# Performance work log

Measured on AMD Instinct MI355X. Metric: run time of the kernel, lower is better.

## Reference

```python
import jax, jax.numpy as jnp
import numpy as np

N, E = 50000, 500000          # nodes per type, edges per message type
F_IN, H, L = 128, 128, 8      # input feat, hidden_size, num_labels
EPS, SLOPE = 1e-5, 0.01       # BatchNorm eps, LeakyReLU slope


def setup_inputs() -> dict:
    key = jax.random.key(0)
    ks = jax.random.split(key, 16)
    s = 0.05
    d = {}
    d["x_n0"] = jax.random.normal(ks[0], (N, F_IN), jnp.float32)
    d["x_n1"] = jax.random.normal(ks[1], (N, F_IN), jnp.float32)
    # stacked per-message-type SAGE params (3 message types), two layers
    d["Wn1"] = jax.random.normal(ks[2], (3, F_IN, H), jnp.float32) * s
    d["Ws1"] = jax.random.normal(ks[3], (3, F_IN, H), jnp.float32) * s
    d["Wu1"] = jax.random.normal(ks[4], (3, 2 * H, H), jnp.float32) * s
    d["Wn2"] = jax.random.normal(ks[5], (3, H, H), jnp.float32) * s
    d["Ws2"] = jax.random.normal(ks[6], (3, H, H), jnp.float32) * s
    d["Wu2"] = jax.random.normal(ks[7], (3, 2 * H, H), jnp.float32) * s
    for nm in ("bn1", "bs1", "bu1", "bn2", "bs2", "bu2"):
        d[nm] = jnp.zeros((3, H), jnp.float32)
    # per-node-type BatchNorm affine params (2 node types), two layers
    d["gamma1"] = jnp.ones((2, H), jnp.float32)
    d["beta1"] = jnp.zeros((2, H), jnp.float32)
    d["gamma2"] = jnp.ones((2, H), jnp.float32)
    d["beta2"] = jnp.zeros((2, H), jnp.float32)
    # per-node-type post-MP linear
    d["Wp"] = jax.random.normal(ks[8], (2, H, L), jnp.float32) * s
    d["bp"] = jnp.zeros((2, L), jnp.float32)
    # edge_index per message type: [2, E] with row0=src, row1=dst
    d["ei0"] = jax.random.randint(ks[9], (2, E), 0, N, jnp.int32)   # n0 -> n1
    d["ei1"] = jax.random.randint(ks[10], (2, E), 0, N, jnp.int32)  # n1 -> n0
    d["ei2"] = jax.random.randint(ks[11], (2, E), 0, N, jnp.int32)  # n0 -> n0
    return d


def _segment_mean(x, idx, n):
    s = jax.ops.segment_sum(x, idx, num_segments=n)
    c = jax.ops.segment_sum(jnp.ones((idx.shape[0], 1), x.dtype), idx, num_segments=n)
    return s / jnp.maximum(c, 1.0)


def _sage(x_src, x_dst, ei, Wn, bn, Ws, bs, Wu, bu):
    # gather source feats per edge, scatter-mean to dst, then linear branches
    agg = _segment_mean(x_src[ei[0]], ei[1], x_dst.shape[0])  # [N_dst, F]
    h = jnp.concatenate([agg @ Wn + bn, x_dst @ Ws + bs], axis=-1)
    return h @ Wu + bu


def _bn(x, g, b):
    m = x.mean(0)
    v = ((x - m) ** 2).mean(0)  # biased variance, as torch BN training mode
    return (x - m) * jax.lax.rsqrt(v + EPS) * g + b


def _lrelu(x):
    return jnp.where(x >= 0, x, SLOPE * x)


def _layer(x0, x1, ei0, ei1, ei2, Wn, bn, Ws, bs, Wu, bu, gamma, beta):
    m0 = _sage(x0, x1, ei0, Wn[0], bn[0], Ws[0], bs[0], Wu[0], bu[0])  # dst n1
    m1 = _sage(x1, x0, ei1, Wn[1], bn[1], Ws[1], bs[1], Wu[1], bu[1])  # dst n0
    m2 = _sage(x0, x0, ei2, Wn[2], bn[2], Ws[2], bs[2], Wu[2], bu[2])  # dst n0
    h0 = 0.5 * (m1 + m2)   # mean over the 2 message types targeting n0
    h1 = m0                # single message type for n1
    h0 = _lrelu(_bn(h0, gamma[0], beta[0]))
    h1 = _lrelu(_bn(h1, gamma[1], beta[1]))
    return h0, h1


def reference(x_n0, x_n1, Wn1, bn1, Ws1, bs1, Wu1, bu1,
              Wn2, bn2, Ws2, bs2, Wu2, bu2,
              gamma1, beta1, gamma2, beta2, Wp, bp, ei0, ei1, ei2):
    h0, h1 = _layer(x_n0, x_n1, ei0, ei1, ei2, Wn1, bn1, Ws1, bs1, Wu1, bu1, gamma1, beta1)
    h0, h1 = _layer(h0, h1, ei0, ei1, ei2, Wn2, bn2, Ws2, bs2, Wu2, bu2, gamma2, beta2)
    out0 = h0 @ Wp[0] + bp[0]
    out1 = h1 @ Wp[1] + bp[1]
    return jnp.stack([out0, out1])  # [2, N, L]
```

## Files before the change

kernel.cpp:

```cpp
#include <hip/hip_runtime.h>

#define LBL 8
#define NBMAX 128
#define BSH 9
#define BCAP 8192

typedef __attribute__((ext_vector_type(8))) short short8;
typedef __attribute__((ext_vector_type(4))) float f32x4;

__device__ __forceinline__ uint f2bf(float x) {
    uint u = __float_as_uint(x);
    return (u + 0x7fffu + ((u >> 16) & 1u)) >> 16;
}
__device__ __forceinline__ float bflo(uint v) { return __uint_as_float(v << 16); }
__device__ __forceinline__ float bfhi(uint v) { return __uint_as_float(v & 0xffff0000u); }

__global__ void f2b2(const float4* __restrict__ x0, const float4* __restrict__ x1,
                     uint2* __restrict__ o0, uint2* __restrict__ o1, int n4) {
    int y = blockIdx.y;
    const float4* in = y ? x1 : x0;
    uint2* out = y ? o1 : o0;
    int i = blockIdx.x * blockDim.x + threadIdx.x;
    int stride = gridDim.x * blockDim.x;
    for (; i < n4; i += stride) {
        float4 v = in[i];
        uint2 o;
        o.x = f2bf(v.x) | (f2bf(v.y) << 16);
        o.y = f2bf(v.z) | (f2bf(v.w) << 16);
        out[i] = o;
    }
}


__global__ void bhist3(const int* __restrict__ e0, const int* __restrict__ e1,
                       const int* __restrict__ e2, int E, int NB, int* __restrict__ bcnt) {
    int m = blockIdx.y;
    const int* dst = (m == 0 ? e0 : (m == 1 ? e1 : e2)) + E;
    __shared__ int h[NBMAX];
    int tid = threadIdx.x;
    if (tid < NB) h[tid] = 0;
    __syncthreads();
    int i = blockIdx.x * blockDim.x + tid, st = gridDim.x * blockDim.x;
    for (; i < E; i += st) atomicAdd(&h[dst[i] >> BSH], 1);
    __syncthreads();
    if (tid < NB && h[tid]) atomicAdd(&bcnt[m * NB + tid], h[tid]);
}

__global__ void bscan(const int* __restrict__ bcnt, int* __restrict__ bso,
                      int* __restrict__ gcur, int NB) {
    int m = threadIdx.x;
    if (m >= 3) return;
    int acc = 0;
    for (int b = 0; b < NB; ++b) {
        bso[m * (NB + 1) + b] = acc;
        gcur[m * NB + b] = acc;
        acc += bcnt[m * NB + b];
    }
    bso[m * (NB + 1) + NB] = acc;
}

#define BIN_CH 16
__global__ __launch_bounds__(256) void bin3(const int* __restrict__ e0, const int* __restrict__ e1,
                                            const int* __restrict__ e2, int E, int NB,
                                            int* __restrict__ gcur, int2* __restrict__ pairs) {
    int m = blockIdx.y;
    const int* eb = (m == 0 ? e0 : (m == 1 ? e1 : e2));
    const int* src = eb;
    const int* dst = eb + E;
    int2* pp = pairs + (size_t)m * E;
    int* gc = gcur + m * NB;
    __shared__ int h[NBMAX], base[NBMAX], pos[NBMAX];
    int tid = threadIdx.x;
    if (tid < NB) { h[tid] = 0; pos[tid] = 0; }
    __syncthreads();
    int i0 = blockIdx.x * (256 * BIN_CH);
    int sv[BIN_CH], dv[BIN_CH], bk[BIN_CH];
    #pragma unroll
    for (int u = 0; u < BIN_CH; ++u) {
        int i = i0 + u * 256 + tid;
        bk[u] = -1;
        if (i < E) {
            sv[u] = src[i];
            dv[u] = dst[i];
            bk[u] = dv[u] >> BSH;
            atomicAdd(&h[bk[u]], 1);
        }
    }
    __syncthreads();
    if (tid < NB && h[tid]) base[tid] = atomicAdd(&gc[tid], h[tid]);
    __syncthreads();
    #pragma unroll
    for (int u = 0; u < BIN_CH; ++u) {
        if (bk[u] >= 0) {
            int p = base[bk[u]] + atomicAdd(&pos[bk[u]], 1);
            pp[p] = make_int2(sv[u], dv[u]);
        }
    }
}

__global__ __launch_bounds__(256) void csr3(const int2* __restrict__ pairs, const int* __restrict__ bso,
                                            int E, int N, int NB,
                                            int* __restrict__ offs, int* __restrict__ srcs) {
    int m = blockIdx.y, b = blockIdx.x;
    const int2* pp = pairs + (size_t)m * E;
    int gstart = bso[m * (NB + 1) + b];
    int gend = bso[m * (NB + 1) + b + 1];
    int cnt = gend - gstart;
    if (cnt > BCAP) cnt = BCAP;
    int d0 = b << BSH;
    int dcnt = N - d0;
    if (dcnt > (1 << BSH)) dcnt = 1 << BSH;

    __shared__ int hist[1 << BSH], po[1 << BSH], off0[1 << BSH];
    __shared__ int lsort[BCAP];
    __shared__ int wsum[4];
    int tid = threadIdx.x;
    hist[tid] = 0;
    hist[tid + 256] = 0;
    __syncthreads();
    for (int i = tid; i < cnt; i += 256) atomicAdd(&hist[pp[gstart + i].y - d0], 1);
    __syncthreads();
    int a = hist[2 * tid], b2 = hist[2 * tid + 1];
    int s = a + b2;
    int lane = tid & 63, w = tid >> 6;
    #pragma unroll
    for (int o = 1; o < 64; o <<= 1) {
        int v = __shfl_up(s, o, 64);
        if (lane >= o) s += v;
    }
    if (lane == 63) wsum[w] = s;
    __syncthreads();
    int wp = 0;
    #pragma unroll
    for (int q = 0; q < 4; ++q)
        if (q < w) wp += wsum[q];
    int excl = wp + s - a - b2;
    off0[2 * tid] = excl; off0[2 * tid + 1] = excl + a;
    po[2 * tid] = excl;   po[2 * tid + 1] = excl + a;
    __syncthreads();
    for (int j = tid; j < dcnt; j += 256) offs[(size_t)m * (N + 1) + d0 + j] = gstart + off0[j];
    if (b == NB - 1 && tid == 0) offs[(size_t)m * (N + 1) + N] = bso[m * (NB + 1) + NB];
    for (int i = tid; i < cnt; i += 256) {
        int2 e = pp[gstart + i];
        int p = atomicAdd(&po[e.y - d0], 1);
        if (p < BCAP) lsort[p] = e.x;
    }
    __syncthreads();
    for (int i = tid; i < cnt; i += 256) srcs[(size_t)m * E + gstart + i] = lsort[i];
}

__global__ void agg3(const ushort* __restrict__ s0, const ushort* __restrict__ s1,
                     const ushort* __restrict__ s2,
                     uint* __restrict__ o0, uint* __restrict__ o1, uint* __restrict__ o2,
                     const int* __restrict__ offs, const int* __restrict__ srcs,
                     int n, int E) {
    int m = blockIdx.y;
    const uint4* x = (const uint4*)(m == 0 ? s0 : (m == 1 ? s1 : s2));
    uint4* o = (uint4*)(m == 0 ? o0 : (m == 1 ? o1 : o2));
    const int* off = offs + (size_t)m * (n + 1);
    const int* sl = srcs + (size_t)m * E;

    int tid = threadIdx.x;
    int l16 = tid & 15;
    int row = blockIdx.x * 16 + (tid >> 4);
    if (row >= n) return;
    int s = off[row], e = off[row + 1];
    float a0 = 0, a1 = 0, a2 = 0, a3 = 0, a4 = 0, a5 = 0, a6 = 0, a7 = 0;
    int i = s;
    for (; i + 1 < e; i += 2) {
        uint4 v0 = x[(size_t)sl[i] * 16 + l16];
        uint4 v1 = x[(size_t)sl[i + 1] * 16 + l16];
        a0 += bflo(v0.x) + bflo(v1.x); a1 += bfhi(v0.x) + bfhi(v1.x);
        a2 += bflo(v0.y) + bflo(v1.y); a3 += bfhi(v0.y) + bfhi(v1.y);
        a4 += bflo(v0.z) + bflo(v1.z); a5 += bfhi(v0.z) + bfhi(v1.z);
        a6 += bflo(v0.w) + bflo(v1.w); a7 += bfhi(v0.w) + bfhi(v1.w);
    }
    if (i < e) {
        uint4 v0 = x[(size_t)sl[i] * 16 + l16];
        a0 += bflo(v0.x); a1 += bfhi(v0.x);
        a2 += bflo(v0.y); a3 += bfhi(v0.y);
        a4 += bflo(v0.z); a5 += bfhi(v0.z);
        a6 += bflo(v0.w); a7 += bfhi(v0.w);
    }
    int d = e - s;
    float inv = 1.f / (float)(d > 0 ? d : 1);
    uint4 r;
    r.x = f2bf(a0 * inv) | (f2bf(a1 * inv) << 16);
    r.y = f2bf(a2 * inv) | (f2bf(a3 * inv) << 16);
    r.z = f2bf(a4 * inv) | (f2bf(a5 * inv) << 16);
    r.w = f2bf(a6 * inv) | (f2bf(a7 * inv) << 16);
    o[(size_t)row * 16 + l16] = r;
}

__global__ void fuseW(const float* __restrict__ Wn1, const float* __restrict__ Ws1,
                      const float* __restrict__ Wu1,
                      const float* __restrict__ Wn2, const float* __restrict__ Ws2,
                      const float* __restrict__ Wu2, ushort* __restrict__ FT) {
    int j5 = blockIdx.y;
    int l = j5 / 5, t = j5 - l * 5;
    const float* Wn = l ? Wn2 : Wn1;
    const float* Ws = l ? Ws2 : Ws1;
    const float* Wu = l ? Wu2 : Wu1;
    const float *A0, *B0, *A1 = nullptr, *B1 = nullptr;
    float al;
    switch (t) {
        case 0: A0 = Wn;          B0 = Wu;          al = 1.0f; break;
        case 1: A0 = Wn + 16384;  B0 = Wu + 32768;  al = 0.5f; break;
        case 2: A0 = Wn + 32768;  B0 = Wu + 65536;  al = 0.5f; break;
        case 3: A0 = Ws;          B0 = Wu + 16384;  al = 1.0f; break;
        default:
            A0 = Ws + 16384; B0 = Wu + 49152;
            A1 = Ws + 32768; B1 = Wu + 81920;
            al = 0.5f; break;
    }
    int i = blockIdx.x, j = threadIdx.x;
    float s0 = 0, s1 = 0, s2 = 0, s3 = 0;
    #pragma unroll 4
    for (int k = 0; k < 128; k += 4) {
        s0 += A0[i * 128 + k]     * B0[k * 128 + j];
        s1 += A0[i * 128 + k + 1] * B0[(k + 1) * 128 + j];
        s2 += A0[i * 128 + k + 2] * B0[(k + 2) * 128 + j];
        s3 += A0[i * 128 + k + 3] * B0[(k + 3) * 128 + j];
    }
    if (A1) {
        #pragma unroll 4
        for (int k = 0; k < 128; k += 4) {
            s0 += A1[i * 128 + k]     * B1[k * 128 + j];
            s1 += A1[i * 128 + k + 1] * B1[(k + 1) * 128 + j];
            s2 += A1[i * 128 + k + 2] * B1[(k + 2) * 128 + j];
            s3 += A1[i * 128 + k + 3] * B1[(k + 3) * 128 + j];
        }
    }
    float r = al * ((s0 + s1) + (s2 + s3));
    FT[(size_t)j5 * 16384 + j * 128 + i] = (ushort)f2bf(r);
}

__global__ void fuseB(const float* __restrict__ bn1, const float* __restrict__ bs1,
                      const float* __restrict__ bu1, const float* __restrict__ Wu1,
                      const float* __restrict__ bn2, const float* __restrict__ bs2,
                      const float* __restrict__ bu2, const float* __restrict__ Wu2,
                      float* __restrict__ FC) {
    int jb = blockIdx.x;
    int l = jb >> 1, which = jb & 1;
    const float* bn = l ? bn2 : bn1;
    const float* bs = l ? bs2 : bs1;
    const float* bu = l ? bu2 : bu1;
    const float* Wu = l ? Wu2 : Wu1;
    int j = threadIdx.x;
    float s = 0.f;
    if (which == 0) {
        s = bu[j];
        for (int k = 0; k < 128; ++k)
            s += bn[k] * Wu[k * 128 + j] + bs[k] * Wu[(128 + k) * 128 + j];
    } else {
        #pragma unroll
        for (int tt = 1; tt <= 2; ++tt) {
            const float* Wt = Wu + tt * 32768;
            float p = bu[tt * 128 + j];
            for (int k = 0; k < 128; ++k)
                p += bn[tt * 128 + k] * Wt[k * 128 + j] + bs[tt * 128 + k] * Wt[(128 + k) * 128 + j];
            s += 0.5f * p;
        }
    }
    FC[jb * 128 + j] = s;
}

__global__ __launch_bounds__(256) void gemm2_mfma(
    const ushort* __restrict__ Aq0, const ushort* __restrict__ Wq0,
    const ushort* __restrict__ Aq1, const ushort* __restrict__ Wq1,
    const ushort* __restrict__ Ap0, const ushort* __restrict__ Wp0,
    const ushort* __restrict__ Ap1, const ushort* __restrict__ Wp1,
    const ushort* __restrict__ Ap2, const ushort* __restrict__ Wp2,
    const float* __restrict__ biasq, const float* __restrict__ biasp,
    ushort* __restrict__ Cq, ushort* __restrict__ Cp, int M,
    float* __restrict__ STW) {
    __shared__ ushort As[64 * 128];
    int y = blockIdx.y;
    const float* bias = y ? biasp : biasq;
    ushort* C = y ? Cp : Cq;
    float* colsum = STW + (size_t)(blockIdx.x & 31) * 512 + (y ? 0 : 256);
    float* colsq = colsum + 128;

    int tid = threadIdx.x;
    int wid = tid >> 6;
    int lane = tid & 63;
    int l15 = lane & 15, lg = lane >> 4;
    int row0 = blockIdx.x * 64;
    int nIn = y ? 3 : 2;

    short8 bw[3][4][2];
    #pragma unroll
    for (int inp = 0; inp < 3; ++inp) {
        const ushort* W = (inp == 0) ? (y ? Wp0 : Wq0)
                        : (inp == 1) ? (y ? Wp1 : Wq1) : Wp2;
        #pragma unroll
        for (int k0 = 0; k0 < 4; ++k0)
            #pragma unroll
            for (int cb = 0; cb < 2; ++cb)
                bw[inp][k0][cb] = *(const short8*)(W + (size_t)(wid * 32 + cb * 16 + l15) * 128 + k0 * 32 + lg * 8);
    }

    f32x4 acc[4][2];
    #pragma unroll
    for (int rb = 0; rb < 4; ++rb)
        #pragma unroll
        for (int cb = 0; cb < 2; ++cb) acc[rb][cb] = (f32x4){0.f, 0.f, 0.f, 0.f};

    int r_ = tid >> 4, ch = tid & 15;
    #pragma unroll
    for (int inp = 0; inp < 3; ++inp) {
        if (inp == 2 && nIn == 2) break;
        const ushort* A = (inp == 0) ? (y ? Ap0 : Aq0)
                        : (inp == 1) ? (y ? Ap1 : Aq1) : Ap2;
        __syncthreads();
        #pragma unroll
        for (int p = 0; p < 4; ++p) {
            int row = p * 16 + r_;
            int gr = row0 + row;
            if (gr > M - 1) gr = M - 1;
            uint4 v = *(const uint4*)(A + (size_t)gr * 128 + ch * 8);
            *(uint4*)&As[row * 128 + ((ch ^ (row & 7)) * 8)] = v;
        }
        __syncthreads();
        #pragma unroll
        for (int k0 = 0; k0 < 4; ++k0) {
            short8 a[4];
            #pragma unroll
            for (int rb = 0; rb < 4; ++rb)
                a[rb] = *(const short8*)&As[(rb * 16 + l15) * 128 + (((k0 * 4 + lg) ^ (l15 & 7)) * 8)];
            #pragma unroll
            for (int rb = 0; rb < 4; ++rb)
                #pragma unroll
                for (int cb = 0; cb < 2; ++cb)
                    acc[rb][cb] = __builtin_amdgcn_mfma_f32_16x16x32_bf16(a[rb], bw[inp][k0][cb], acc[rb][cb], 0, 0, 0);
        }
    }

    float ps[2] = {0.f, 0.f}, pq[2] = {0.f, 0.f};
    int colbase = wid * 32;
    #pragma unroll
    for (int cb = 0; cb < 2; ++cb) {
        int col = colbase + cb * 16 + l15;
        float b = bias[col];
        #pragma unroll
        for (int rb = 0; rb < 4; ++rb) {
            int rbase = row0 + rb * 16 + lg * 4;
            #pragma unroll
            for (int i = 0; i < 4; ++i) {
                int r = rbase + i;
                if (r < M) {
                    float v = acc[rb][cb][i] + b;
                    C[(size_t)r * 128 + col] = (ushort)f2bf(v);
                    ps[cb] += v;
                    pq[cb] += v * v;
                }
            }
        }
    }
    #pragma unroll
    for (int cb = 0; cb < 2; ++cb) {
        ps[cb] += __shfl_xor(ps[cb], 16, 64);
        ps[cb] += __shfl_xor(ps[cb], 32, 64);
        pq[cb] += __shfl_xor(pq[cb], 16, 64);
        pq[cb] += __shfl_xor(pq[cb], 32, 64);
    }
    if (lane < 16) {
        atomicAdd(&colsum[colbase + lane], ps[0]);
        atomicAdd(&colsq[colbase + lane], pq[0]);
        atomicAdd(&colsum[colbase + 16 + lane], ps[1]);
        atomicAdd(&colsq[colbase + 16 + lane], pq[1]);
    }
}

__global__ void bn_fin2(float* __restrict__ STW, float* __restrict__ ST,
                        const float* __restrict__ g0, const float* __restrict__ b0,
                        const float* __restrict__ g1, const float* __restrict__ b1, int N) {
    int tid = threadIdx.x;
    int which = tid >> 7, c = tid & 127;
    float s = 0.f, q = 0.f;
    #pragma unroll 8
    for (int cp = 0; cp < 32; ++cp) {
        s += STW[(size_t)cp * 512 + which * 256 + c];
        q += STW[(size_t)cp * 512 + which * 256 + 128 + c];
    }
    #pragma unroll 8
    for (int cp = 0; cp < 32; ++cp) {
        STW[(size_t)cp * 512 + which * 256 + c] = 0.f;
        STW[(size_t)cp * 512 + which * 256 + 128 + c] = 0.f;
    }
    const float* g = which ? g1 : g0;
    const float* b = which ? b1 : b0;
    float m = s / (float)N;
    float v = q / (float)N - m * m;
    float rs = rsqrtf(v + 1e-5f);
    float sc = g[c] * rs;
    ST[512 + which * 256 + c] = sc;
    ST[640 + which * 256 + c] = b[c] - m * sc;
}

__global__ void bn_apply2(const ushort* __restrict__ Cp, ushort* __restrict__ X0b,
                          const ushort* __restrict__ Cq, ushort* __restrict__ X1b,
                          const float* __restrict__ ST, int n4) {
    int y = blockIdx.y;
    const uint2* in = (const uint2*)(y ? Cq : Cp);
    uint2* out = (uint2*)(y ? X1b : X0b);
    const float* sc = ST + 512 + y * 256;
    const float* sh = sc + 128;
    int i = blockIdx.x * blockDim.x + threadIdx.x;
    int stride = gridDim.x * blockDim.x;
    for (; i < n4; i += stride) {
        uint2 v = in[i];
        int cb = (i * 4) & 127;
        float4 s4 = *(const float4*)&sc[cb];
        float4 h4 = *(const float4*)&sh[cb];
        float y0 = bflo(v.x) * s4.x + h4.x;
        float y1 = bfhi(v.x) * s4.y + h4.y;
        float y2 = bflo(v.y) * s4.z + h4.z;
        float y3 = bfhi(v.y) * s4.w + h4.w;
        y0 = (y0 >= 0.f) ? y0 : 0.01f * y0;
        y1 = (y1 >= 0.f) ? y1 : 0.01f * y1;
        y2 = (y2 >= 0.f) ? y2 : 0.01f * y2;
        y3 = (y3 >= 0.f) ? y3 : 0.01f * y3;
        uint2 o;
        o.x = f2bf(y0) | (f2bf(y1) << 16);
        o.y = f2bf(y2) | (f2bf(y3) << 16);
        out[i] = o;
    }
}

__global__ void projbn2(const ushort* __restrict__ Cp, const ushort* __restrict__ Cq,
                        const float* __restrict__ ST,
                        const float* __restrict__ Wp, const float* __restrict__ bp,
                        float* __restrict__ out, int N) {
    int y = blockIdx.y;
    const uint* h = (const uint*)(y ? Cq : Cp);
    const float* W = Wp + y * 1024;
    const float* b = bp + y * 8;
    float* op = out + (size_t)y * N * 8;
    __shared__ float Wsh[1024];
    __shared__ float scs[128], shs[128];
    __shared__ float bsh[8];
    int tid = threadIdx.x;
    for (int i = tid; i < 1024; i += 256) Wsh[i] = W[i];
    if (tid < 128) {
        scs[tid] = ST[512 + y * 256 + tid];
        shs[tid] = ST[640 + y * 256 + tid];
    }
    if (tid < 8) bsh[tid] = b[tid];
    __syncthreads();
    int idx = blockIdx.x * 256 + tid;
    if (idx >= N * LBL) return;
    int r = idx >> 3, c = idx & 7;
    const uint* hr = h + (size_t)r * 64;
    float s = bsh[c];
    #pragma unroll
    for (int k2 = 0; k2 < 64; ++k2) {
        uint v = hr[k2];
        float xa = bflo(v) * scs[2 * k2] + shs[2 * k2];
        float xb = bfhi(v) * scs[2 * k2 + 1] + shs[2 * k2 + 1];
        xa = (xa >= 0.f) ? xa : 0.01f * xa;
        xb = (xb >= 0.f) ? xb : 0.01f * xb;
        s += xa * Wsh[(2 * k2) * 8 + c] + xb * Wsh[(2 * k2 + 1) * 8 + c];
    }
    op[idx] = s;
}


extern "C" void kernel_launch(void* const* d_in, const int* in_sizes, int n_in,
                              void* d_out, int out_size, void* d_ws, size_t ws_size,
                              hipStream_t stream) {
    const float* x0 = (const float*)d_in[0];
    const float* x1 = (const float*)d_in[1];
    const float* Wn1 = (const float*)d_in[2];
    const float* Ws1 = (const float*)d_in[3];
    const float* Wu1 = (const float*)d_in[4];
    const float* Wn2 = (const float*)d_in[5];
    const float* Ws2 = (const float*)d_in[6];
    const float* Wu2 = (const float*)d_in[7];
    const float* bnn[2] = {(const float*)d_in[8], (const float*)d_in[11]};
    const float* bss[2] = {(const float*)d_in[9], (const float*)d_in[12]};
    const float* buu[2] = {(const float*)d_in[10], (const float*)d_in[13]};
    const float* gam[2] = {(const float*)d_in[14], (const float*)d_in[16]};
    const float* bet[2] = {(const float*)d_in[15], (const float*)d_in[17]};
    const float* Wp = (const float*)d_in[18];
    const float* bp = (const float*)d_in[19];
    const int* ei[3] = {(const int*)d_in[20], (const int*)d_in[21], (const int*)d_in[22]};

    const int N = in_sizes[0] / 128;
    const int E = in_sizes[20] / 2;
    const int NB = (N + (1 << BSH) - 1) >> BSH;
    float* out = (float*)d_out;

    char* wp_ = (char*)d_ws;
    auto carve = [&](size_t bytes) {
        char* r = wp_;
        wp_ += (bytes + 255) & ~(size_t)255;
        return r;
    };
    size_t nodeB = (size_t)N * 128 * sizeof(ushort);
    ushort* Cp = (ushort*)carve(nodeB);
    ushort* Cq = (ushort*)carve(nodeB);
    ushort* Pb = (ushort*)carve(nodeB);
    ushort* Rb = (ushort*)carve(nodeB);
    ushort* Sb = (ushort*)carve(nodeB);
    ushort* X0b = (ushort*)carve(nodeB);
    ushort* X1b = (ushort*)carve(nodeB);
    ushort* x0b = (ushort*)carve(nodeB);
    ushort* x1b = (ushort*)carve(nodeB);
    ushort* FT = (ushort*)carve(10 * 16384 * 2);
    float* FC = (float*)carve(4 * 128 * 4);
    float* ST = (float*)carve(1024 * 4);
    float* STW = (float*)carve(32 * 512 * 4);
    int* offs = (int*)carve((size_t)3 * (N + 1) * 4);
    int* srcs = (int*)carve((size_t)3 * E * 4);
    int* bcnt = (int*)carve((size_t)3 * NB * 4);
    int* bso = (int*)carve((size_t)3 * (NB + 1) * 4);
    int* gcur = (int*)carve((size_t)3 * NB * 4);
    int2* pairs = (int2*)Cp;

    const int ag = (N + 15) / 16;
    const int gg = (N + 63) / 64;
    const int pg = (N * LBL + 255) / 256;
    const int bg = (E + 256 * BIN_CH - 1) / (256 * BIN_CH);

    f2b2<<<dim3(1024, 2), 256, 0, stream>>>((const float4*)x0, (const float4*)x1,
                                            (uint2*)x0b, (uint2*)x1b, N * 32);

    hipMemsetAsync(bcnt, 0, (size_t)3 * NB * 4, stream);
    hipMemsetAsync(STW, 0, 32 * 512 * 4, stream);
    bhist3<<<dim3(512, 3), 256, 0, stream>>>(ei[0], ei[1], ei[2], E, NB, bcnt);
    bscan<<<1, 64, 0, stream>>>(bcnt, bso, gcur, NB);
    bin3<<<dim3(bg, 3), 256, 0, stream>>>(ei[0], ei[1], ei[2], E, NB, gcur, pairs);
    csr3<<<dim3(NB, 3), 256, 0, stream>>>(pairs, bso, E, N, NB, offs, srcs);

    fuseW<<<dim3(128, 10), 128, 0, stream>>>(Wn1, Ws1, Wu1, Wn2, Ws2, Wu2, FT);
    fuseB<<<4, 128, 0, stream>>>(bnn[0], bss[0], buu[0], Wu1, bnn[1], bss[1], buu[1], Wu2, FC);

    const ushort* srcS[2][3] = {{x0b, x1b, x0b}, {X0b, X1b, X0b}};
    const ushort* dstX[2][2] = {{x0b, x1b}, {X0b, X1b}};

    for (int l = 0; l < 2; ++l) {
        const ushort* FA0T = FT + (size_t)(l * 5 + 0) * 16384;
        const ushort* FA1T = FT + (size_t)(l * 5 + 1) * 16384;
        const ushort* FA2T = FT + (size_t)(l * 5 + 2) * 16384;
        const ushort* FB1T = FT + (size_t)(l * 5 + 3) * 16384;
        const ushort* FB0T = FT + (size_t)(l * 5 + 4) * 16384;
        const float* fcH1 = FC + (l * 2 + 0) * 128;
        const float* fcH0 = FC + (l * 2 + 1) * 128;

        agg3<<<dim3(ag, 3), 256, 0, stream>>>(srcS[l][0], srcS[l][1], srcS[l][2],
                                              (uint*)Pb, (uint*)Rb, (uint*)Sb,
                                              offs, srcs, N, E);

        gemm2_mfma<<<dim3(gg, 2), 256, 0, stream>>>(
            Pb, FA0T, dstX[l][1], FB1T,
            Rb, FA1T, Sb, FA2T, dstX[l][0], FB0T,
            fcH1, fcH0, Cq, Cp, N, STW);

        bn_fin2<<<1, 256, 0, stream>>>(STW, ST, gam[l], bet[l], gam[l] + 128, bet[l] + 128, N);
        if (l == 0)
            bn_apply2<<<dim3(1024, 2), 256, 0, stream>>>(Cp, X0b, Cq, X1b, ST, N * 32);
    }

    projbn2<<<dim3(pg, 2), 256, 0, stream>>>(Cp, Cq, ST, Wp, bp, out, N);
}
```

Before: 316.0 us.

## Fuse neighbor mean-aggregation into the SAGE MFMA GEMM kernel

Removes the separate agg3 kernel and performs the CSR gather-mean directly into the GEMM's shared-memory A tile. This avoids writing three aggregated node buffers to global memory and reading them back, and saves one launch per layer. The gather loop is unrolled by 4 for more loads in flight, and weight fragments are loaded per input so fewer registers are live. The gather now runs at GEMM occupancy with only 64 rows per block, which may expose more memory latency than the standalone aggregation kernel did.

```diff
diff --git a/kernel.cpp b/kernel.cpp
--- a/kernel.cpp
+++ b/kernel.cpp
@@ -147,49 +147,6 @@
     }
     __syncthreads();
     for (int i = tid; i < cnt; i += 256) srcs[(size_t)m * E + gstart + i] = lsort[i];
-}
-
-__global__ void agg3(const ushort* __restrict__ s0, const ushort* __restrict__ s1,
-                     const ushort* __restrict__ s2,
-                     uint* __restrict__ o0, uint* __restrict__ o1, uint* __restrict__ o2,
-                     const int* __restrict__ offs, const int* __restrict__ srcs,
-                     int n, int E) {
-    int m = blockIdx.y;
-    const uint4* x = (const uint4*)(m == 0 ? s0 : (m == 1 ? s1 : s2));
-    uint4* o = (uint4*)(m == 0 ? o0 : (m == 1 ? o1 : o2));
-    const int* off = offs + (size_t)m * (n + 1);
-    const int* sl = srcs + (size_t)m * E;
-
-    int tid = threadIdx.x;
-    int l16 = tid & 15;
-    int row = blockIdx.x * 16 + (tid >> 4);
-    if (row >= n) return;
-    int s = off[row], e = off[row + 1];
-    float a0 = 0, a1 = 0, a2 = 0, a3 = 0, a4 = 0, a5 = 0, a6 = 0, a7 = 0;
-    int i = s;
-    for (; i + 1 < e; i += 2) {
-        uint4 v0 = x[(size_t)sl[i] * 16 + l16];
-        uint4 v1 = x[(size_t)sl[i + 1] * 16 + l16];
-        a0 += bflo(v0.x) + bflo(v1.x); a1 += bfhi(v0.x) + bfhi(v1.x);
-        a2 += bflo(v0.y) + bflo(v1.y); a3 += bfhi(v0.y) + bfhi(v1.y);
-        a4 += bflo(v0.z) + bflo(v1.z); a5 += bfhi(v0.z) + bfhi(v1.z);
-        a6 += bflo(v0.w) + bflo(v1.w); a7 += bfhi(v0.w) + bfhi(v1.w);
-    }
-    if (i < e) {
-        uint4 v0 = x[(size_t)sl[i] * 16 + l16];
-        a0 += bflo(v0.x); a1 += bfhi(v0.x);
-        a2 += bflo(v0.y); a3 += bfhi(v0.y);
-        a4 += bflo(v0.z); a5 += bfhi(v0.z);
-        a6 += bflo(v0.w); a7 += bfhi(v0.w);
-    }
-    int d = e - s;
-    float inv = 1.f / (float)(d > 0 ? d : 1);
-    uint4 r;
-    r.x = f2bf(a0 * inv) | (f2bf(a1 * inv) << 16);
-    r.y = f2bf(a2 * inv) | (f2bf(a3 * inv) << 16);
-    r.z = f2bf(a4 * inv) | (f2bf(a5 * inv) << 16);
-    r.w = f2bf(a6 * inv) | (f2bf(a7 * inv) << 16);
-    o[(size_t)row * 16 + l16] = r;
 }
 
 __global__ void fuseW(const float* __restrict__ Wn1, const float* __restrict__ Ws1,
@@ -265,14 +222,14 @@
     FC[jb * 128 + j] = s;
 }
 
-__global__ __launch_bounds__(256) void gemm2_mfma(
-    const ushort* __restrict__ Aq0, const ushort* __restrict__ Wq0,
-    const ushort* __restrict__ Aq1, const ushort* __restrict__ Wq1,
-    const ushort* __restrict__ Ap0, const ushort* __restrict__ Wp0,
-    const ushort* __restrict__ Ap1, const ushort* __restrict__ Wp1,
-    const ushort* __restrict__ Ap2, const ushort* __restrict__ Wp2,
+__global__ __launch_bounds__(256) void sage_fused(
+    const ushort* __restrict__ Gq, const ushort* __restrict__ Dq,
+    const ushort* __restrict__ Gp0, const ushort* __restrict__ Gp1,
+    const ushort* __restrict__ Dp,
+    const ushort* __restrict__ FTl,
+    const int* __restrict__ offs, const int* __restrict__ srcs, int E, int M,
     const float* __restrict__ biasq, const float* __restrict__ biasp,
-    ushort* __restrict__ Cq, ushort* __restrict__ Cp, int M,
+    ushort* __restrict__ Cq, ushort* __restrict__ Cp,
     float* __restrict__ STW) {
     __shared__ ushort As[64 * 128];
     int y = blockIdx.y;
@@ -286,40 +243,84 @@
     int lane = tid & 63;
     int l15 = lane & 15, lg = lane >> 4;
     int row0 = blockIdx.x * 64;
-    int nIn = y ? 3 : 2;
-
-    short8 bw[3][4][2];
+    int rloc = tid >> 4, ch = tid & 15;
+
+    f32x4 acc[4][2];
+    #pragma unroll
+    for (int rb = 0; rb < 4; ++rb)
+        #pragma unroll
+        for (int cb = 0; cb < 2; ++cb) acc[rb][cb] = (f32x4){0.f, 0.f, 0.f, 0.f};
+
     #pragma unroll
     for (int inp = 0; inp < 3; ++inp) {
-        const ushort* W = (inp == 0) ? (y ? Wp0 : Wq0)
-                        : (inp == 1) ? (y ? Wp1 : Wq1) : Wp2;
+        if (inp == 2 && y == 0) break;
+        int t = (y == 0) ? (inp == 0 ? 0 : 3) : (inp == 2 ? 4 : inp + 1);
+        bool gath = (y == 0) ? (inp == 0) : (inp < 2);
+        const ushort* W = FTl + (size_t)t * 16384;
+
+        short8 bw[4][2];
         #pragma unroll
         for (int k0 = 0; k0 < 4; ++k0)
             #pragma unroll
             for (int cb = 0; cb < 2; ++cb)
-                bw[inp][k0][cb] = *(const short8*)(W + (size_t)(wid * 32 + cb * 16 + l15) * 128 + k0 * 32 + lg * 8);
-    }
-
-    f32x4 acc[4][2];
-    #pragma unroll
-    for (int rb = 0; rb < 4; ++rb)
-        #pragma unroll
-        for (int cb = 0; cb < 2; ++cb) acc[rb][cb] = (f32x4){0.f, 0.f, 0.f, 0.f};
-
-    int r_ = tid >> 4, ch = tid & 15;
-    #pragma unroll
-    for (int inp = 0; inp < 3; ++inp) {
-        if (inp == 2 && nIn == 2) break;
-        const ushort* A = (inp == 0) ? (y ? Ap0 : Aq0)
-                        : (inp == 1) ? (y ? Ap1 : Aq1) : Ap2;
+                bw[k0][cb] = *(const short8*)(W + (size_t)(wid * 32 + cb * 16 + l15) * 128 + k0 * 32 + lg * 8);
+
         __syncthreads();
-        #pragma unroll
-        for (int p = 0; p < 4; ++p) {
-            int row = p * 16 + r_;
-            int gr = row0 + row;
-            if (gr > M - 1) gr = M - 1;
-            uint4 v = *(const uint4*)(A + (size_t)gr * 128 + ch * 8);
-            *(uint4*)&As[row * 128 + ((ch ^ (row & 7)) * 8)] = v;
+        if (gath) {
+            int m = (y == 0) ? 0 : inp + 1;
+            const uint4* xs = (const uint4*)((y == 0) ? Gq : (inp == 0 ? Gp0 : Gp1));
+            const int* off = offs + (size_t)m * (M + 1);
+            const int* sl = srcs + (size_t)m * E;
+            #pragma unroll 1
+            for (int p = 0; p < 4; ++p) {
+                int row = p * 16 + rloc;
+                int gr = row0 + row;
+                uint4 r = make_uint4(0, 0, 0, 0);
+                if (gr < M) {
+                    int s = off[gr], e = off[gr + 1];
+                    float a0 = 0, a1 = 0, a2 = 0, a3 = 0, a4 = 0, a5 = 0, a6 = 0, a7 = 0;
+                    int i = s;
+                    for (; i + 3 < e; i += 4) {
+                        int j0 = sl[i], j1 = sl[i + 1], j2 = sl[i + 2], j3 = sl[i + 3];
+                        uint4 v0 = xs[(size_t)j0 * 16 + ch];
+                        uint4 v1 = xs[(size_t)j1 * 16 + ch];
+                        uint4 v2 = xs[(size_t)j2 * 16 + ch];
+                        uint4 v3 = xs[(size_t)j3 * 16 + ch];
+                        a0 += (bflo(v0.x) + bflo(v1.x)) + (bflo(v2.x) + bflo(v3.x));
+                        a1 += (bfhi(v0.x) + bfhi(v1.x)) + (bfhi(v2.x) + bfhi(v3.x));
+                        a2 += (bflo(v0.y) + bflo(v1.y)) + (bflo(v2.y) + bflo(v3.y));
+                        a3 += (bfhi(v0.y) + bfhi(v1.y)) + (bfhi(v2.y) + bfhi(v3.y));
+                        a4 += (bflo(v0.z) + bflo(v1.z)) + (bflo(v2.z) + bflo(v3.z));
+                        a5 += (bfhi(v0.z) + bfhi(v1.z)) + (bfhi(v2.z) + bfhi(v3.z));
+                        a6 += (bflo(v0.w) + bflo(v1.w)) + (bflo(v2.w) + bflo(v3.w));
+                        a7 += (bfhi(v0.w) + bfhi(v1.w)) + (bfhi(v2.w) + bfhi(v3.w));
+                    }
+                    for (; i < e; ++i) {
+                        uint4 v = xs[(size_t)sl[i] * 16 + ch];
+                        a0 += bflo(v.x); a1 += bfhi(v.x);
+                        a2 += bflo(v.y); a3 += bfhi(v.y);
+                        a4 += bflo(v.z); a5 += bfhi(v.z);
+                        a6 += bflo(v.w); a7 += bfhi(v.w);
+                    }
+                    int d = e - s;
+                    float inv = 1.f / (float)(d > 0 ? d : 1);
+                    r.x = f2bf(a0 * inv) | (f2bf(a1 * inv) << 16);
+                    r.y = f2bf(a2 * inv) | (f2bf(a3 * inv) << 16);
+                    r.z = f2bf(a4 * inv) | (f2bf(a5 * inv) << 16);
+                    r.w = f2bf(a6 * inv) | (f2bf(a7 * inv) << 16);
+                }
+                *(uint4*)&As[row * 128 + ((ch ^ (row & 7)) * 8)] = r;
+            }
+        } else {
+            const ushort* dsrc = (y == 0) ? Dq : Dp;
+            #pragma unroll
+            for (int p = 0; p < 4; ++p) {
+                int row = p * 16 + rloc;
+                int gr = row0 + row;
+                if (gr > M - 1) gr = M - 1;
+                uint4 v = *(const uint4*)(dsrc + (size_t)gr * 128 + ch * 8);
+                *(uint4*)&As[row * 128 + ((ch ^ (row & 7)) * 8)] = v;
+            }
         }
         __syncthreads();
         #pragma unroll
@@ -332,7 +333,7 @@
             for (int rb = 0; rb < 4; ++rb)
                 #pragma unroll
                 for (int cb = 0; cb < 2; ++cb)
-                    acc[rb][cb] = __builtin_amdgcn_mfma_f32_16x16x32_bf16(a[rb], bw[inp][k0][cb], acc[rb][cb], 0, 0, 0);
+                    acc[rb][cb] = __builtin_amdgcn_mfma_f32_16x16x32_bf16(a[rb], bw[k0][cb], acc[rb][cb], 0, 0, 0);
         }
     }
 
@@ -500,9 +501,6 @@
     size_t nodeB = (size_t)N * 128 * sizeof(ushort);
     ushort* Cp = (ushort*)carve(nodeB);
     ushort* Cq = (ushort*)carve(nodeB);
-    ushort* Pb = (ushort*)carve(nodeB);
-    ushort* Rb = (ushort*)carve(nodeB);
-    ushort* Sb = (ushort*)carve(nodeB);
     ushort* X0b = (ushort*)carve(nodeB);
     ushort* X1b = (ushort*)carve(nodeB);
     ushort* x0b = (ushort*)carve(nodeB);
@@ -518,7 +516,6 @@
     int* gcur = (int*)carve((size_t)3 * NB * 4);
     int2* pairs = (int2*)Cp;
 
-    const int ag = (N + 15) / 16;
     const int gg = (N + 63) / 64;
     const int pg = (N * LBL + 255) / 256;
     const int bg = (E + 256 * BIN_CH - 1) / (256 * BIN_CH);
@@ -540,22 +537,15 @@
     const ushort* dstX[2][2] = {{x0b, x1b}, {X0b, X1b}};
 
     for (int l = 0; l < 2; ++l) {
-        const ushort* FA0T = FT + (size_t)(l * 5 + 0) * 16384;
-        const ushort* FA1T = FT + (size_t)(l * 5 + 1) * 16384;
-        const ushort* FA2T = FT + (size_t)(l * 5 + 2) * 16384;
-        const ushort* FB1T = FT + (size_t)(l * 5 + 3) * 16384;
-        const ushort* FB0T = FT + (size_t)(l * 5 + 4) * 16384;
+        const ushort* FTl = FT + (size_t)l * 5 * 16384;
         const float* fcH1 = FC + (l * 2 + 0) * 128;
         const float* fcH0 = FC + (l * 2 + 1) * 128;
 
-        agg3<<<dim3(ag, 3), 256, 0, stream>>>(srcS[l][0], srcS[l][1], srcS[l][2],
-                                              (uint*)Pb, (uint*)Rb, (uint*)Sb,
-                                              offs, srcs, N, E);
-
-        gemm2_mfma<<<dim3(gg, 2), 256, 0, stream>>>(
-            Pb, FA0T, dstX[l][1], FB1T,
-            Rb, FA1T, Sb, FA2T, dstX[l][0], FB0T,
-            fcH1, fcH0, Cq, Cp, N, STW);
+        sage_fused<<<dim3(gg, 2), 256, 0, stream>>>(
+            srcS[l][0], dstX[l][1],
+            srcS[l][1], srcS[l][2], dstX[l][0],
+            FTl, offs, srcs, E, N,
+            fcH1, fcH0, Cq, Cp, STW);
 
         bn_fin2<<<1, 256, 0, stream>>>(STW, ST, gam[l], bet[l], gam[l] + 128, bet[l] + 128, N);
         if (l == 0)
```

Result: slower. 413.0 us (+30.7%).
